# Kernel optimization log

Hardware: AMD Instinct MI355X
Metric: run time of the kernel (lower is better)

## Reference

```python
import jax, jax.numpy as jnp
import numpy as np

C = 512
NUM_HEADS = 8
HEAD_DIM = C // NUM_HEADS


def setup_inputs() -> dict:
    key = jax.random.key(0)
    ks = jax.random.split(key, 5)
    B, H, W = 4, 48, 48
    x = jax.random.normal(ks[0], (B, C, H, W), dtype=jnp.float32)
    # 1x1 conv weights == dense matrices over channel dim
    Wqkv = jax.random.normal(ks[1], (3 * C, C), dtype=jnp.float32) * (1.0 / np.sqrt(C))
    bqkv = jax.random.normal(ks[2], (3 * C,), dtype=jnp.float32) * 0.01
    Wout = jax.random.normal(ks[3], (C, C), dtype=jnp.float32) * (1.0 / np.sqrt(C))
    bout = jax.random.normal(ks[4], (C,), dtype=jnp.float32) * 0.01
    return {"x": x, "Wqkv": Wqkv, "bqkv": bqkv, "Wout": Wout, "bout": bout}


def reference(x, Wqkv, bqkv, Wout, bout):
    B, Cc, H, W = x.shape
    S = H * W
    # qkv 1x1 conv: [B, 3C, H, W] -> reshape (B, 3, heads, head_dim, S)
    qkv = jnp.einsum('bchw,oc->bohw', x, Wqkv) + bqkv[None, :, None, None]
    qkv = qkv.reshape(B, 3, NUM_HEADS, HEAD_DIM, S)
    q, k, v = qkv[:, 0], qkv[:, 1], qkv[:, 2]  # [B, h, d, S]
    # tokens along S: q^T k, scaled softmax
    scale = HEAD_DIM ** -0.5
    attn = jnp.einsum('bhds,bhdt->bhst', q, k) * scale  # [B, h, S, S]
    attn = jax.nn.softmax(attn, axis=-1)
    out = jnp.einsum('bhst,bhdt->bhds', attn, v)  # [B, h, d, S]
    out = out.reshape(B, Cc, H, W)
    out = jnp.einsum('bchw,oc->bohw', out, Wout) + bout[None, :, None, None]
    return out
```

## Files before the change

### kernel.cpp

```cpp
#include <hip/hip_runtime.h>

#define S_LEN 2304
#define CDIM  512
#define NHEAD 8

typedef __attribute__((ext_vector_type(4)))  float f32x4;
typedef __attribute__((ext_vector_type(16))) float f32x16;
typedef __attribute__((ext_vector_type(8)))  _Float16 f16x8;
typedef __attribute__((ext_vector_type(2)))  __fp16 fp16x2r;
typedef _Float16 h16;

#define QSCALE 0.18033688011112042f

__device__ __forceinline__ float fexp2(float x) {
#if __has_builtin(__builtin_amdgcn_exp2f)
    return __builtin_amdgcn_exp2f(x);
#else
    return exp2f(x);
#endif
}

__device__ __forceinline__ unsigned cvtpk(float a, float b) {
    union { fp16x2r v; unsigned u; } c;
    c.v = __builtin_amdgcn_cvt_pkrtz(a, b);
    return c.u;
}

__device__ __forceinline__ void gll16(const h16* g, h16* l) {
    __builtin_amdgcn_global_load_lds(
        (const __attribute__((address_space(1))) unsigned int*)g,
        (__attribute__((address_space(3))) unsigned int*)l, 16, 0, 0);
}

__global__ __launch_bounds__(256) void prep(
    const float* __restrict__ x, h16* __restrict__ xT,
    const float* __restrict__ Wq, const float* __restrict__ Wo,
    h16* __restrict__ Wq_h, h16* __restrict__ Wo_h)
{
    const int bid = blockIdx.x;
    if (bid >= 1152) {
        const int NQ = 1536 * 512;
        const int NO = 512 * 512;
        int i = ((bid - 1152) * 256 + threadIdx.x) * 4;
        if (i >= NQ + NO) return;
        float4 v;
        h16* dst;
        if (i < NQ) { v = *(const float4*)(Wq + i);        dst = Wq_h + i; }
        else        { v = *(const float4*)(Wo + (i - NQ)); dst = Wo_h + (i - NQ); }
        union { h16 h[4]; uint2 u; } pk;
        pk.h[0]=(h16)v.x; pk.h[1]=(h16)v.y; pk.h[2]=(h16)v.z; pk.h[3]=(h16)v.w;
        *(uint2*)dst = pk.u;
        return;
    }
    const int s0 = (bid % 36) * 64;
    const int c0 = ((bid / 36) & 7) * 64;
    const int b  = bid / 288;
    __shared__ h16 Ts[64][76];

    const int t  = threadIdx.x;
    const int cq = t >> 4;
    const int sq = t & 15;

    const float* xb = x + ((size_t)b * CDIM + c0 + cq * 4) * S_LEN + s0 + sq * 4;
    float4 r0 = *(const float4*)(xb);
    float4 r1 = *(const float4*)(xb + S_LEN);
    float4 r2 = *(const float4*)(xb + 2 * S_LEN);
    float4 r3 = *(const float4*)(xb + 3 * S_LEN);

    union { h16 h[4]; uint2 u; } pk;
    pk.h[0]=(h16)r0.x; pk.h[1]=(h16)r1.x; pk.h[2]=(h16)r2.x; pk.h[3]=(h16)r3.x;
    *(uint2*)&Ts[sq*4+0][cq*4] = pk.u;
    pk.h[0]=(h16)r0.y; pk.h[1]=(h16)r1.y; pk.h[2]=(h16)r2.y; pk.h[3]=(h16)r3.y;
    *(uint2*)&Ts[sq*4+1][cq*4] = pk.u;
    pk.h[0]=(h16)r0.z; pk.h[1]=(h16)r1.z; pk.h[2]=(h16)r2.z; pk.h[3]=(h16)r3.z;
    *(uint2*)&Ts[sq*4+2][cq*4] = pk.u;
    pk.h[0]=(h16)r0.w; pk.h[1]=(h16)r1.w; pk.h[2]=(h16)r2.w; pk.h[3]=(h16)r3.w;
    *(uint2*)&Ts[sq*4+3][cq*4] = pk.u;

    __syncthreads();
    const int s  = t >> 2;
    const int cc = (t & 3) * 16;
    uint2 a0 = *(uint2*)&Ts[s][cc + 0];
    uint2 a1 = *(uint2*)&Ts[s][cc + 4];
    uint2 a2 = *(uint2*)&Ts[s][cc + 8];
    uint2 a3 = *(uint2*)&Ts[s][cc + 12];
    h16* dst = xT + ((size_t)b * S_LEN + s0 + s) * CDIM + c0 + cc;
    uint4 w0 = make_uint4(a0.x, a0.y, a1.x, a1.y);
    uint4 w1 = make_uint4(a2.x, a2.y, a3.x, a3.y);
    *(uint4*)dst       = w0;
    *(uint4*)(dst + 8) = w1;
}

__global__ __launch_bounds__(256) void gemm_qkv(
    const h16* __restrict__ Wh, const float* __restrict__ bqkv,
    const h16* __restrict__ xT, h16* __restrict__ qT, h16* __restrict__ kT,
    h16* __restrict__ vN)
{
    const int n0 = blockIdx.x * 128;
    const int m0 = blockIdx.y * 128;
    const int b  = blockIdx.z;
    __shared__ h16 Ws[128 * 64];
    __shared__ h16 Xs[128 * 64];

    const int tid = threadIdx.x;
    const int lid = tid & 63, w = tid >> 6;
    const int g = lid >> 4, ln = lid & 15;
    const int wm = w & 1, wn = w >> 1;
    const int srow = lid >> 3;
    const int sblk = (lid & 7) ^ (srow & 7);

    f32x4 acc[4][4];
#pragma unroll
    for (int i = 0; i < 4; i++)
#pragma unroll
        for (int j = 0; j < 4; j++) acc[i][j] = (f32x4)0.f;

    const h16* Wbase = Wh + (size_t)m0 * CDIM;
    const h16* Xbase = xT + ((size_t)b * S_LEN + n0) * CDIM;
    const bool vblk = (m0 >= 1024);

    for (int kt = 0; kt < CDIM; kt += 64) {
        __syncthreads();
#pragma unroll
        for (int i = 0; i < 4; i++) {
            const int row0 = w * 32 + i * 8;
            gll16(Wbase + (size_t)(row0 + srow) * CDIM + kt + sblk * 8, &Ws[row0 * 64]);
            gll16(Xbase + (size_t)(row0 + srow) * CDIM + kt + sblk * 8, &Xs[row0 * 64]);
        }
        __syncthreads();

#pragma unroll
        for (int kc = 0; kc < 2; kc++) {
            f16x8 af[4], bf[4];
#pragma unroll
            for (int i = 0; i < 4; i++) {
                const int ra = wm * 64 + i * 16 + ln;
                const int ca = (kc * 64 + g * 16) ^ ((ra & 7) << 4);
                af[i] = *(const f16x8*)&Ws[ra * 64 + ca / 2];
                const int rb = wn * 64 + i * 16 + ln;
                const int cb = (kc * 64 + g * 16) ^ ((rb & 7) << 4);
                bf[i] = *(const f16x8*)&Xs[rb * 64 + cb / 2];
            }
            if (!vblk) {
#pragma unroll
                for (int i = 0; i < 4; i++)
#pragma unroll
                    for (int j = 0; j < 4; j++)
                        acc[i][j] = __builtin_amdgcn_mfma_f32_16x16x32_f16(
                            af[i], bf[j], acc[i][j], 0, 0, 0);
            } else {
#pragma unroll
                for (int i = 0; i < 4; i++)
#pragma unroll
                    for (int j = 0; j < 4; j++)
                        acc[i][j] = __builtin_amdgcn_mfma_f32_16x16x32_f16(
                            bf[i], af[j], acc[i][j], 0, 0, 0);
            }
        }
    }

    if (!vblk) {
#pragma unroll
        for (int i = 0; i < 4; i++) {
            const int mb = m0 + wm * 64 + i * 16 + 4 * g;
            const float4 bv = *(const float4*)&bqkv[mb];
            const int mloc = mb & 511;
            const int hh = mloc >> 6, d0 = mloc & 63;
            const bool isq = (mb < 512);
            const float scl = isq ? QSCALE : 1.0f;
            h16* base = (isq ? qT : kT);
#pragma unroll
            for (int j = 0; j < 4; j++) {
                const int n = n0 + wn * 64 + j * 16 + ln;
                union { h16 h[4]; uint2 u; } pk;
                pk.h[0] = (h16)((acc[i][j][0] + bv.x) * scl);
                pk.h[1] = (h16)((acc[i][j][1] + bv.y) * scl);
                pk.h[2] = (h16)((acc[i][j][2] + bv.z) * scl);
                pk.h[3] = (h16)((acc[i][j][3] + bv.w) * scl);
                *(uint2*)(base + (((size_t)b * 8 + hh) * S_LEN + n) * 64 + d0) = pk.u;
            }
        }
    } else {
#pragma unroll
        for (int j = 0; j < 4; j++) {
            const int m = m0 + wm * 64 + j * 16 + ln;
            const float bias = bqkv[m];
            const int mloc = m - 1024;
            const int hh = mloc >> 6, d = mloc & 63;
            h16* base = vN + (((size_t)b * 8 + hh) * 64 + d) * S_LEN;
#pragma unroll
            for (int i = 0; i < 4; i++) {
                const int nb = n0 + wn * 64 + i * 16 + 4 * g;
                union { h16 h[4]; uint2 u; } pk;
                pk.h[0] = (h16)(acc[i][j][0] + bias);
                pk.h[1] = (h16)(acc[i][j][1] + bias);
                pk.h[2] = (h16)(acc[i][j][2] + bias);
                pk.h[3] = (h16)(acc[i][j][3] + bias);
                *(uint2*)(base + nb) = pk.u;
            }
        }
    }
}

__global__ __launch_bounds__(192, 4) void attn_f16(
    const h16* __restrict__ qT, const h16* __restrict__ kT,
    const h16* __restrict__ vN, h16* __restrict__ attT)
{
    const int f    = blockIdx.x;
    const int xcd  = f & 7;
    const int slot = f >> 3;
    const int bh   = xcd + 8 * (slot / 24);
    const int x    = slot % 24;
    const int b    = bh >> 3;
    const int h    = bh & 7;
    const int s0   = x * 96;

    __shared__ h16 Ks[2][64 * 64];
    __shared__ h16 Vs[2][64 * 64];

    const int tid = threadIdx.x;
    const int lid = tid & 63, w = tid >> 6;
    const int l31 = lid & 31, hi = lid >> 5;
    const int srow = lid >> 3;
    const int sblk = (lid & 7) ^ (srow & 7);

    const h16* qb = qT + ((size_t)b * 8 + h) * S_LEN * 64;
    const h16* kb = kT + ((size_t)b * 8 + h) * S_LEN * 64;
    const h16* vb = vN + ((size_t)b * 8 + h) * 64 * S_LEN;

    const int sq = s0 + w * 32 + l31;

    f16x8 qf[4];
    {
        const h16* qrow = qb + (size_t)sq * 64;
#pragma unroll
        for (int ds = 0; ds < 4; ds++)
            qf[ds] = *(const f16x8*)(qrow + ds * 16 + hi * 8);
    }

    f16x8 ones;
#pragma unroll
    for (int i = 0; i < 8; i++) ones[i] = (h16)1.0f;

    for (int c = w; c < 8; c += 3)
        gll16(kb + (size_t)(c * 8 + srow) * 64 + sblk * 8, &Ks[0][c * 8 * 64]);
    __syncthreads();

    float m_run = -1e30f;
    f32x16 oacc0 = (f32x16)0.f, oacc1 = (f32x16)0.f, lacc = (f32x16)0.f;
    f16x8 pf_prev[4];

    const int NT = S_LEN / 64;
    for (int i = 0; i < NT; i++) {
        const int kcur = i & 1;
        if (i + 1 < NT) {
            const int kt1 = (i + 1) * 64;
            for (int c = w; c < 8; c += 3)
                gll16(kb + (size_t)(kt1 + c * 8 + srow) * 64 + sblk * 8,
                      &Ks[kcur ^ 1][c * 8 * 64]);
        }
        {
            const int kt0 = i * 64;
            for (int c = w; c < 8; c += 3)
                gll16(vb + (size_t)(c * 8 + srow) * S_LEN + kt0 + sblk * 8,
                      &Vs[i & 1][c * 8 * 64]);
        }

        const h16* Kc = Ks[kcur];

        f32x16 sacc0 = (f32x16)0.f, sacc1 = (f32x16)0.f;
        __builtin_amdgcn_s_setprio(1);
#pragma unroll
        for (int ds = 0; ds < 4; ds++) {
            const int bc = 2 * ds + hi;
            {
                const int row = l31;
                f16x8 kf = *(const f16x8*)&Kc[row * 64 + ((bc ^ (row & 7)) * 8)];
                sacc0 = __builtin_amdgcn_mfma_f32_32x32x16_f16(kf, qf[ds], sacc0, 0, 0, 0);
            }
            {
                const int row = 32 + l31;
                f16x8 kf = *(const f16x8*)&Kc[row * 64 + ((bc ^ (row & 7)) * 8)];
                sacc1 = __builtin_amdgcn_mfma_f32_32x32x16_f16(kf, qf[ds], sacc1, 0, 0, 0);
            }
        }
        if (i > 0) {
            const h16* Vp = Vs[(i - 1) & 1];
#pragma unroll
            for (int j = 0; j < 4; j++) {
                const int bc = 2 * j + hi;
                lacc = __builtin_amdgcn_mfma_f32_32x32x16_f16(ones, pf_prev[j], lacc, 0, 0, 0);
                {
                    const int row = l31;
                    f16x8 vf = *(const f16x8*)&Vp[row * 64 + ((bc ^ (row & 7)) * 8)];
                    oacc0 = __builtin_amdgcn_mfma_f32_32x32x16_f16(vf, pf_prev[j], oacc0, 0, 0, 0);
                }
                {
                    const int row = 32 + l31;
                    f16x8 vf = *(const f16x8*)&Vp[row * 64 + ((bc ^ (row & 7)) * 8)];
                    oacc1 = __builtin_amdgcn_mfma_f32_32x32x16_f16(vf, pf_prev[j], oacc1, 0, 0, 0);
                }
            }
        }
        __builtin_amdgcn_s_setprio(0);

        float ma = sacc0[0], mb2 = sacc1[0];
#pragma unroll
        for (int r = 1; r < 15; r += 2) {
            ma  = fmaxf(fmaxf(ma,  sacc0[r]), sacc0[r + 1]);
            mb2 = fmaxf(fmaxf(mb2, sacc1[r]), sacc1[r + 1]);
        }
        ma  = fmaxf(ma,  sacc0[15]);
        mb2 = fmaxf(mb2, sacc1[15]);
        float mloc = fmaxf(ma, mb2);
        mloc = fmaxf(mloc, __shfl_xor(mloc, 32));

        if (!__all(mloc <= m_run + 8.0f)) {
            const float mnew = fmaxf(m_run, mloc);
            const float resc = fexp2(m_run - mnew);
#pragma unroll
            for (int r = 0; r < 16; r++) {
                oacc0[r] *= resc; oacc1[r] *= resc; lacc[r] *= resc;
            }
            m_run = mnew;
        }

#pragma unroll
        for (int r = 0; r < 16; r++) sacc0[r] = fexp2(sacc0[r] - m_run);
#pragma unroll
        for (int r = 0; r < 16; r++) sacc1[r] = fexp2(sacc1[r] - m_run);

#pragma unroll
        for (int j = 0; j < 4; j++) {
            const int bse = (j & 1) * 8;
            float pv[8];
#pragma unroll
            for (int r = 0; r < 8; r++)
                pv[r] = (j < 2) ? sacc0[bse + r] : sacc1[bse + r];
            unsigned X0 = cvtpk(pv[0], pv[1]);
            unsigned X1 = cvtpk(pv[2], pv[3]);
            unsigned Y0 = cvtpk(pv[4], pv[5]);
            unsigned Y1 = cvtpk(pv[6], pv[7]);
            asm("v_permlane32_swap_b32 %0, %1" : "+v"(X0), "+v"(Y0));
            asm("v_permlane32_swap_b32 %0, %1" : "+v"(X1), "+v"(Y1));
            union { unsigned u[4]; f16x8 v; } pkk;
            pkk.u[0] = X0; pkk.u[1] = X1; pkk.u[2] = Y0; pkk.u[3] = Y1;
            pf_prev[j] = pkk.v;
        }
        __syncthreads();
    }

    {
        const h16* Vp = Vs[(NT - 1) & 1];
#pragma unroll
        for (int j = 0; j < 4; j++) {
            const int bc = 2 * j + hi;
            lacc = __builtin_amdgcn_mfma_f32_32x32x16_f16(ones, pf_prev[j], lacc, 0, 0, 0);
            {
                const int row = l31;
                f16x8 vf = *(const f16x8*)&Vp[row * 64 + ((bc ^ (row & 7)) * 8)];
                oacc0 = __builtin_amdgcn_mfma_f32_32x32x16_f16(vf, pf_prev[j], oacc0, 0, 0, 0);
            }
            {
                const int row = 32 + l31;
                f16x8 vf = *(const f16x8*)&Vp[row * 64 + ((bc ^ (row & 7)) * 8)];
                oacc1 = __builtin_amdgcn_mfma_f32_32x32x16_f16(vf, pf_prev[j], oacc1, 0, 0, 0);
            }
        }
    }

    const float inv = 1.0f / lacc[0];
    h16* ob = attT + ((size_t)b * S_LEN + sq) * CDIM + h * 64;
#pragma unroll
    for (int gi = 0; gi < 4; gi++) {
        union { h16 hh[4]; uint2 u; } p0, p1;
#pragma unroll
        for (int r = 0; r < 4; r++) {
            p0.hh[r] = (h16)(oacc0[gi * 4 + r] * inv);
            p1.hh[r] = (h16)(oacc1[gi * 4 + r] * inv);
        }
        *(uint2*)(ob + 8 * gi + 4 * hi)      = p0.u;
        *(uint2*)(ob + 32 + 8 * gi + 4 * hi) = p1.u;
    }
}

__global__ __launch_bounds__(256) void gemm_out(
    const h16* __restrict__ attT, const h16* __restrict__ Wh,
    const float* __restrict__ bout, float* __restrict__ out)
{
    const int n0 = blockIdx.x * 64;
    const int m0 = blockIdx.y * 128;
    const int b  = blockIdx.z;
    __shared__ h16 Ws[128 * 64];
    __shared__ h16 Xs[64 * 64];

    const int tid = threadIdx.x;
    const int lid = tid & 63, w = tid >> 6;
    const int g = lid >> 4, ln = lid & 15;
    const int wm = w & 1, wn = w >> 1;
    const int srow = lid >> 3;
    const int sblk = (lid & 7) ^ (srow & 7);

    f32x4 acc[2][4];
#pragma unroll
    for (int i = 0; i < 2; i++)
#pragma unroll
        for (int j = 0; j < 4; j++) acc[i][j] = (f32x4)0.f;

    const h16* Wbase = Wh + (size_t)m0 * CDIM;
    const h16* Xbase = attT + ((size_t)b * S_LEN + n0) * CDIM;

    for (int kt = 0; kt < CDIM; kt += 64) {
        __syncthreads();
#pragma unroll
        for (int i = 0; i < 4; i++) {
            const int row0 = w * 32 + i * 8;
            gll16(Wbase + (size_t)(row0 + srow) * CDIM + kt + sblk * 8, &Ws[row0 * 64]);
        }
#pragma unroll
        for (int i = 0; i < 2; i++) {
            const int row0 = w * 16 + i * 8;
            if (row0 < 64)
                gll16(Xbase + (size_t)(row0 + srow) * CDIM + kt + sblk * 8, &Xs[row0 * 64]);
        }
        __syncthreads();

#pragma unroll
        for (int kc = 0; kc < 2; kc++) {
            f16x8 af[4], bf[2];
#pragma unroll
            for (int j = 0; j < 4; j++) {
                const int ra = wm * 64 + j * 16 + ln;
                const int ca = (kc * 64 + g * 16) ^ ((ra & 7) << 4);
                af[j] = *(const f16x8*)&Ws[ra * 64 + ca / 2];
            }
#pragma unroll
            for (int i = 0; i < 2; i++) {
                const int rb = wn * 32 + i * 16 + ln;
                const int cb = (kc * 64 + g * 16) ^ ((rb & 7) << 4);
                bf[i] = *(const f16x8*)&Xs[rb * 64 + cb / 2];
            }
#pragma unroll
            for (int i = 0; i < 2; i++)
#pragma unroll
                for (int j = 0; j < 4; j++)
                    acc[i][j] = __builtin_amdgcn_mfma_f32_16x16x32_f16(
                        bf[i], af[j], acc[i][j], 0, 0, 0);
        }
    }

#pragma unroll
    for (int j = 0; j < 4; j++) {
        const int m = m0 + wm * 64 + j * 16 + ln;
        const float bias = bout[m];
        float* base = out + ((size_t)b * CDIM + m) * S_LEN;
#pragma unroll
        for (int i = 0; i < 2; i++) {
            const int nb = n0 + wn * 32 + i * 16 + 4 * g;
            float4 o;
            o.x = acc[i][j][0] + bias;
            o.y = acc[i][j][1] + bias;
            o.z = acc[i][j][2] + bias;
            o.w = acc[i][j][3] + bias;
            *(float4*)(base + nb) = o;
        }
    }
}

extern "C" void kernel_launch(void* const* d_in, const int* in_sizes, int n_in,
                              void* d_out, int out_size, void* d_ws, size_t ws_size,
                              hipStream_t stream)
{
    const float* x    = (const float*)d_in[0];
    const float* Wqkv = (const float*)d_in[1];
    const float* bqkv = (const float*)d_in[2];
    const float* Wout = (const float*)d_in[3];
    const float* bout = (const float*)d_in[4];
    float* out = (float*)d_out;

    h16* xT   = (h16*)d_ws;
    h16* Wq_h = xT   + (size_t)4 * S_LEN * CDIM;
    h16* Wo_h = Wq_h + (size_t)1536 * 512;
    h16* qT   = Wo_h + (size_t)512 * 512;
    h16* kT   = qT   + (size_t)4 * 8 * S_LEN * 64;
    h16* vN   = kT   + (size_t)4 * 8 * S_LEN * 64;
    h16* attT = vN   + (size_t)4 * 8 * S_LEN * 64;

    prep    <<<2176,            256, 0, stream>>>(x, xT, Wqkv, Wout, Wq_h, Wo_h);
    gemm_qkv<<<dim3(18, 12, 4), 256, 0, stream>>>(Wq_h, bqkv, xT, qT, kT, vN);
    attn_f16<<<768,             192, 0, stream>>>(qT, kT, vN, attT);
    gemm_out<<<dim3(36, 4, 4),  256, 0, stream>>>(attT, Wo_h, bout, out);
}
```

Before: 136.4 us.

## Restructure attention kernel with triple-buffered K/V staging and 4-wave blocks

Reworks the attention kernel to use 4 waves per block (128 queries) instead of 3 (96 queries), and triple-buffers K and V tiles with explicit vmcnt waits and raw barriers instead of double-buffering and __syncthreads. The PV product is now computed in the same iteration rather than deferred by one. The row-sum is kept as a scalar accumulated from the exponentials with a cross-half shuffle, replacing the ones-matrix MFMA. The aim is to cut MFMA work and barrier stalls and to deepen load prefetch. In exchange it uses more LDS, drops the setprio hints, and loses the overlap of PV with the next tile's QK.

New measurement: 129.2 us. -5.3%, faster.

```diff
diff --git a/kernel.cpp b/kernel.cpp
--- a/kernel.cpp
+++ b/kernel.cpp
@@ -202,21 +202,21 @@
     }
 }
 
-__global__ __launch_bounds__(192, 4) void attn_f16(
+__global__ __launch_bounds__(256, 3) void attn_f16(
     const h16* __restrict__ qT, const h16* __restrict__ kT,
     const h16* __restrict__ vN, h16* __restrict__ attT)
 {
     const int f    = blockIdx.x;
     const int xcd  = f & 7;
     const int slot = f >> 3;
-    const int bh   = xcd + 8 * (slot / 24);
-    const int x    = slot % 24;
+    const int bh   = xcd + 8 * (slot / 18);
+    const int x    = slot % 18;
     const int b    = bh >> 3;
     const int h    = bh & 7;
-    const int s0   = x * 96;
-
-    __shared__ h16 Ks[2][64 * 64];
-    __shared__ h16 Vs[2][64 * 64];
+    const int s0   = x * 128;
+
+    __shared__ h16 Ks[3][64 * 64];
+    __shared__ h16 Vs[3][64 * 64];
 
     const int tid = threadIdx.x;
     const int lid = tid & 63, w = tid >> 6;
@@ -238,38 +238,37 @@
             qf[ds] = *(const f16x8*)(qrow + ds * 16 + hi * 8);
     }
 
-    f16x8 ones;
-#pragma unroll
-    for (int i = 0; i < 8; i++) ones[i] = (h16)1.0f;
-
-    for (int c = w; c < 8; c += 3)
-        gll16(kb + (size_t)(c * 8 + srow) * 64 + sblk * 8, &Ks[0][c * 8 * 64]);
-    __syncthreads();
-
-    float m_run = -1e30f;
-    f32x16 oacc0 = (f32x16)0.f, oacc1 = (f32x16)0.f, lacc = (f32x16)0.f;
-    f16x8 pf_prev[4];
+    auto stage = [&](int t, int buf) {
+        const int kt = t * 64;
+        for (int c = w; c < 16; c += 4) {
+            if (c < 8)
+                gll16(kb + (size_t)(kt + c * 8 + srow) * 64 + sblk * 8,
+                      &Ks[buf][c * 8 * 64]);
+            else
+                gll16(vb + (size_t)((c - 8) * 8 + srow) * S_LEN + kt + sblk * 8,
+                      &Vs[buf][(c - 8) * 8 * 64]);
+        }
+    };
+
+    stage(0, 0);
+    stage(1, 1);
+    asm volatile("s_waitcnt vmcnt(4)" ::: "memory");
+    __builtin_amdgcn_sched_barrier(0);
+    __builtin_amdgcn_s_barrier();
+    __builtin_amdgcn_sched_barrier(0);
+
+    float m_run = -1e30f, l_run = 0.f;
+    f32x16 oacc0 = (f32x16)0.f, oacc1 = (f32x16)0.f;
 
     const int NT = S_LEN / 64;
     for (int i = 0; i < NT; i++) {
-        const int kcur = i & 1;
-        if (i + 1 < NT) {
-            const int kt1 = (i + 1) * 64;
-            for (int c = w; c < 8; c += 3)
-                gll16(kb + (size_t)(kt1 + c * 8 + srow) * 64 + sblk * 8,
-                      &Ks[kcur ^ 1][c * 8 * 64]);
-        }
-        {
-            const int kt0 = i * 64;
-            for (int c = w; c < 8; c += 3)
-                gll16(vb + (size_t)(c * 8 + srow) * S_LEN + kt0 + sblk * 8,
-                      &Vs[i & 1][c * 8 * 64]);
-        }
-
-        const h16* Kc = Ks[kcur];
+        const int cur = i % 3;
+        if (i + 2 < NT) stage(i + 2, (i + 2) % 3);
+
+        const h16* Kc = Ks[cur];
+        const h16* Vc = Vs[cur];
 
         f32x16 sacc0 = (f32x16)0.f, sacc1 = (f32x16)0.f;
-        __builtin_amdgcn_s_setprio(1);
 #pragma unroll
         for (int ds = 0; ds < 4; ds++) {
             const int bc = 2 * ds + hi;
@@ -284,25 +283,6 @@
                 sacc1 = __builtin_amdgcn_mfma_f32_32x32x16_f16(kf, qf[ds], sacc1, 0, 0, 0);
             }
         }
-        if (i > 0) {
-            const h16* Vp = Vs[(i - 1) & 1];
-#pragma unroll
-            for (int j = 0; j < 4; j++) {
-                const int bc = 2 * j + hi;
-                lacc = __builtin_amdgcn_mfma_f32_32x32x16_f16(ones, pf_prev[j], lacc, 0, 0, 0);
-                {
-                    const int row = l31;
-                    f16x8 vf = *(const f16x8*)&Vp[row * 64 + ((bc ^ (row & 7)) * 8)];
-                    oacc0 = __builtin_amdgcn_mfma_f32_32x32x16_f16(vf, pf_prev[j], oacc0, 0, 0, 0);
-                }
-                {
-                    const int row = 32 + l31;
-                    f16x8 vf = *(const f16x8*)&Vp[row * 64 + ((bc ^ (row & 7)) * 8)];
-                    oacc1 = __builtin_amdgcn_mfma_f32_32x32x16_f16(vf, pf_prev[j], oacc1, 0, 0, 0);
-                }
-            }
-        }
-        __builtin_amdgcn_s_setprio(0);
 
         float ma = sacc0[0], mb2 = sacc1[0];
 #pragma unroll
@@ -319,17 +299,23 @@
             const float mnew = fmaxf(m_run, mloc);
             const float resc = fexp2(m_run - mnew);
 #pragma unroll
-            for (int r = 0; r < 16; r++) {
-                oacc0[r] *= resc; oacc1[r] *= resc; lacc[r] *= resc;
-            }
+            for (int r = 0; r < 16; r++) { oacc0[r] *= resc; oacc1[r] *= resc; }
+            l_run *= resc;
             m_run = mnew;
         }
 
-#pragma unroll
-        for (int r = 0; r < 16; r++) sacc0[r] = fexp2(sacc0[r] - m_run);
-#pragma unroll
-        for (int r = 0; r < 16; r++) sacc1[r] = fexp2(sacc1[r] - m_run);
-
+        float lsum = 0.f;
+#pragma unroll
+        for (int r = 0; r < 16; r++) {
+            sacc0[r] = fexp2(sacc0[r] - m_run); lsum += sacc0[r];
+        }
+#pragma unroll
+        for (int r = 0; r < 16; r++) {
+            sacc1[r] = fexp2(sacc1[r] - m_run); lsum += sacc1[r];
+        }
+        l_run += lsum + __shfl_xor(lsum, 32);
+
+        f16x8 pf[4];
 #pragma unroll
         for (int j = 0; j < 4; j++) {
             const int bse = (j & 1) * 8;
@@ -345,31 +331,37 @@
             asm("v_permlane32_swap_b32 %0, %1" : "+v"(X1), "+v"(Y1));
             union { unsigned u[4]; f16x8 v; } pkk;
             pkk.u[0] = X0; pkk.u[1] = X1; pkk.u[2] = Y0; pkk.u[3] = Y1;
-            pf_prev[j] = pkk.v;
-        }
-        __syncthreads();
-    }
-
-    {
-        const h16* Vp = Vs[(NT - 1) & 1];
+            pf[j] = pkk.v;
+        }
+
 #pragma unroll
         for (int j = 0; j < 4; j++) {
             const int bc = 2 * j + hi;
-            lacc = __builtin_amdgcn_mfma_f32_32x32x16_f16(ones, pf_prev[j], lacc, 0, 0, 0);
             {
                 const int row = l31;
-                f16x8 vf = *(const f16x8*)&Vp[row * 64 + ((bc ^ (row & 7)) * 8)];
-                oacc0 = __builtin_amdgcn_mfma_f32_32x32x16_f16(vf, pf_prev[j], oacc0, 0, 0, 0);
+                f16x8 vf = *(const f16x8*)&Vc[row * 64 + ((bc ^ (row & 7)) * 8)];
+                oacc0 = __builtin_amdgcn_mfma_f32_32x32x16_f16(vf, pf[j], oacc0, 0, 0, 0);
             }
             {
                 const int row = 32 + l31;
-                f16x8 vf = *(const f16x8*)&Vp[row * 64 + ((bc ^ (row & 7)) * 8)];
-                oacc1 = __builtin_amdgcn_mfma_f32_32x32x16_f16(vf, pf_prev[j], oacc1, 0, 0, 0);
-            }
-        }
-    }
-
-    const float inv = 1.0f / lacc[0];
+                f16x8 vf = *(const f16x8*)&Vc[row * 64 + ((bc ^ (row & 7)) * 8)];
+                oacc1 = __builtin_amdgcn_mfma_f32_32x32x16_f16(vf, pf[j], oacc1, 0, 0, 0);
+            }
+        }
+
+        if (i < NT - 1) {
+            if (i + 2 < NT) {
+                asm volatile("s_waitcnt vmcnt(4)" ::: "memory");
+            } else {
+                asm volatile("s_waitcnt vmcnt(0)" ::: "memory");
+            }
+            __builtin_amdgcn_sched_barrier(0);
+            __builtin_amdgcn_s_barrier();
+            __builtin_amdgcn_sched_barrier(0);
+        }
+    }
+
+    const float inv = 1.0f / l_run;
     h16* ob = attT + ((size_t)b * S_LEN + sq) * CDIM + h * 64;
 #pragma unroll
     for (int gi = 0; gi < 4; gi++) {
@@ -488,6 +480,6 @@
 
     prep    <<<2176,            256, 0, stream>>>(x, xT, Wqkv, Wout, Wq_h, Wo_h);
     gemm_qkv<<<dim3(18, 12, 4), 256, 0, stream>>>(Wq_h, bqkv, xT, qT, kT, vN);
-    attn_f16<<<768,             192, 0, stream>>>(qT, kT, vN, attT);
+    attn_f16<<<576,             256, 0, stream>>>(qT, kT, vN, attT);
     gemm_out<<<dim3(36, 4, 4),  256, 0, stream>>>(attT, Wo_h, bout, out);
 }
```
